# Kernel tuning notes

Hardware: AMD Instinct MI355X
Metric: run time of the kernel (lower is better)

Reference implementation:

```python
import jax, jax.numpy as jnp
import numpy as np

N = 50000      # nodes
E = 800000     # edges
D_IN = 128     # in_channels == hidden_channels
D_H = 128
R = 4          # num_relations
L = 3          # n_layers
D_MID = D_H // 4
D_OUT = 40
BN_EPS = 1e-5


def setup_inputs() -> dict:
    key = jax.random.key(0)
    ks = jax.random.split(key, 12)
    return {
        "x": jax.random.normal(ks[0], (N, D_IN), dtype=jnp.float32),
        "edge_index": jax.random.randint(ks[1], (2, E), 0, N, dtype=jnp.int64),
        "edge_type": jax.random.randint(ks[2], (E,), 0, R, dtype=jnp.int64),
        "W_skip": jax.random.normal(ks[3], (L, D_IN, D_H), dtype=jnp.float32) * 0.1,
        "W_film_skip": jax.random.normal(ks[4], (L, D_IN, 2 * D_H), dtype=jnp.float32) * 0.1,
        "W_rel": jax.random.normal(ks[5], (L, R, D_IN, D_H), dtype=jnp.float32) * 0.1,
        "W_film": jax.random.normal(ks[6], (L, R, D_IN, 2 * D_H), dtype=jnp.float32) * 0.1,
        "bn_w": jnp.ones((L, D_H), dtype=jnp.float32),
        "bn_b": jnp.zeros((L, D_H), dtype=jnp.float32),
        "lin1_w": jax.random.normal(ks[7], (D_H, D_MID), dtype=jnp.float32) * 0.1,
        "lin1_b": jnp.zeros((D_MID,), dtype=jnp.float32),
        "lin2_w": jax.random.normal(ks[8], (D_MID, D_OUT), dtype=jnp.float32) * 0.1,
        "lin2_b": jnp.zeros((D_OUT,), dtype=jnp.float32),
    }


def _film_conv(x, Wsk, Wfsk, Wr, Wf, src, dst, etype):
    # Self path: FiLM-modulated skip transform (PyG FiLMConv, act=ReLU).
    beta_s, gamma_s = jnp.split(x @ Wfsk, 2, axis=-1)  # split order: beta, gamma
    out = jax.nn.relu(gamma_s * (x @ Wsk) + beta_s)    # [N, D_H]
    # Per-relation node transforms (small GEMMs, avoids dynamic edge masking).
    xr = jnp.einsum('ni,rio->nro', x, Wr)              # [N, R, D_H]
    bg = jnp.einsum('ni,rio->nro', x, Wf)              # [N, R, 2*D_H]
    beta, gamma = jnp.split(bg, 2, axis=-1)            # each [N, R, D_H]
    # Messages: gamma_i * (W_r x_j) + beta_i, relation chosen per edge.
    msg = jax.nn.relu(gamma[dst, etype] * xr[src, etype] + beta[dst, etype])  # [E, D_H]
    # Mean aggregation per (target node, relation) subgraph, then sum relations.
    seg = dst * R + etype
    sums = jax.ops.segment_sum(msg, seg, num_segments=N * R)
    cnts = jax.ops.segment_sum(jnp.ones((msg.shape[0],), msg.dtype), seg, num_segments=N * R)
    mean = sums / jnp.maximum(cnts, 1.0)[:, None]      # [N*R, D_H]
    return out + mean.reshape(N, R, D_H).sum(axis=1)


def _batchnorm(h, w, b):
    mu = h.mean(axis=0)
    var = ((h - mu) ** 2).mean(axis=0)  # biased variance, as torch BN training
    return (h - mu) * jax.lax.rsqrt(var + BN_EPS) * w + b


def reference(x, edge_index, edge_type, W_skip, W_film_skip, W_rel, W_film,
              bn_w, bn_b, lin1_w, lin1_b, lin2_w, lin2_b):
    src, dst = edge_index[0], edge_index[1]
    h = x
    for l in range(L):
        h = _film_conv(h, W_skip[l], W_film_skip[l], W_rel[l], W_film[l], src, dst, edge_type)
        h = _batchnorm(h, bn_w[l], bn_b[l])
        # dropout treated as identity (deterministic reference)
    h = jax.nn.leaky_relu(h @ lin1_w + lin1_b, negative_slope=0.2)
    return h @ lin2_w + lin2_b
```

## Files before the change

### kernel.cpp

```cpp
#include <hip/hip_runtime.h>

#define N_NODES 50000
#define N_EDGES 800000
#define D 128
#define R_REL 4
#define L_LAYERS 3
#define M_SEG (N_NODES * R_REL)
#define NCOLS 384
#define BN_EPS 1e-5f

typedef unsigned short u16;
typedef __attribute__((ext_vector_type(8))) short short8v;
typedef __attribute__((ext_vector_type(4))) float f32x4;

static __device__ __forceinline__ u16 f2b(float f) {
    union { float f; unsigned int u; } a; a.f = f;
    unsigned int u = a.u;
    return (u16)((u + 0x7FFFu + ((u >> 16) & 1u)) >> 16);
}
static __device__ __forceinline__ float b2f(u16 b) {
    union { unsigned int u; float f; } a; a.u = ((unsigned int)b) << 16;
    return a.f;
}

__global__ void pack_w(const float* __restrict__ Wsk, const float* __restrict__ Wfsk,
                       const float* __restrict__ Wr, const float* __restrict__ Wf,
                       u16* __restrict__ Wpb) {
    int idx = blockIdx.x * 256 + threadIdx.x;
    if (idx >= L_LAYERS * 5 * NCOLS * D) return;
    int k = idx & 127;
    int rem = idx >> 7;
    int j = rem % NCOLS;
    int lp = rem / NCOLS;
    int l = lp / 5, p = lp % 5;
    float v;
    if (p == 0) {
        v = (j < D) ? Wsk[(l * D + k) * D + j] : Wfsk[(l * D + k) * 2 * D + (j - D)];
    } else {
        int r = p - 1;
        v = (j < D) ? Wr[((l * R_REL + r) * D + k) * D + j]
                    : Wf[((l * R_REL + r) * D + k) * 2 * D + (j - D)];
    }
    Wpb[idx] = f2b(v);
}

__global__ void cvt_bf16(const float* __restrict__ x, u16* __restrict__ xb) {
    int idx = blockIdx.x * 256 + threadIdx.x;
    if (idx >= N_NODES * D) return;
    xb[idx] = f2b(x[idx]);
}

__global__ void hist_k(const int* __restrict__ dst, const int* __restrict__ et, int* __restrict__ cnt) {
    int e = blockIdx.x * 256 + threadIdx.x;
    if (e >= N_EDGES) return;
    atomicAdd(&cnt[dst[e] * R_REL + et[e]], 1);
}

__global__ void scan_a(const int* __restrict__ cnt, int* __restrict__ bsum) {
    __shared__ int sm[256];
    int t = threadIdx.x;
    int idx = blockIdx.x * 256 + t;
    sm[t] = (idx < M_SEG) ? cnt[idx] : 0;
    __syncthreads();
    for (int s = 128; s > 0; s >>= 1) {
        if (t < s) sm[t] += sm[t + s];
        __syncthreads();
    }
    if (t == 0) bsum[blockIdx.x] = sm[0];
}

#define NB_SCAN 782
__global__ void scan_b(const int* __restrict__ bsum, int* __restrict__ bsumex, int* __restrict__ offs) {
    __shared__ int sm[1024];
    int t = threadIdx.x;
    int v = (t < NB_SCAN) ? bsum[t] : 0;
    sm[t] = v;
    __syncthreads();
    for (int d = 1; d < 1024; d <<= 1) {
        int add = (t >= d) ? sm[t - d] : 0;
        __syncthreads();
        sm[t] += add;
        __syncthreads();
    }
    if (t < NB_SCAN) bsumex[t] = sm[t] - v;
    if (t == NB_SCAN - 1) offs[M_SEG] = sm[t];
}

__global__ void scan_c(const int* __restrict__ cnt, const int* __restrict__ bsumex, int* __restrict__ offs) {
    __shared__ int sm[256];
    int t = threadIdx.x;
    int idx = blockIdx.x * 256 + t;
    int v = (idx < M_SEG) ? cnt[idx] : 0;
    sm[t] = v;
    __syncthreads();
    for (int d = 1; d < 256; d <<= 1) {
        int add = (t >= d) ? sm[t - d] : 0;
        __syncthreads();
        sm[t] += add;
        __syncthreads();
    }
    if (idx < M_SEG) offs[idx] = bsumex[blockIdx.x] + sm[t] - v;
}

__global__ void scatter_k(const int* __restrict__ src, const int* __restrict__ dst,
                          const int* __restrict__ et, const int* __restrict__ offs,
                          int* __restrict__ tmp, int* __restrict__ esrc) {
    int e = blockIdx.x * 256 + threadIdx.x;
    if (e >= N_EDGES) return;
    int seg = dst[e] * R_REL + et[e];
    int pos = offs[seg] + atomicAdd(&tmp[seg], 1);
    esrc[pos] = src[e];
}

__global__ __launch_bounds__(512) void gemm_mfma(const uint4* __restrict__ Aq,
                                                 const uint4* __restrict__ Bq,
                                                 u16* __restrict__ C) {
    __shared__ uint4 As[128 * 16];
    __shared__ uint4 Bs[128 * 16];
    int t = threadIdx.x;
    int m0 = blockIdx.x * 128;
    int n0 = blockIdx.y * 128;
#pragma unroll
    for (int i = 0; i < 4; ++i) {
        int idx = i * 512 + t;
        int row = idx >> 4, kk = idx & 15;
        int gr = m0 + row;
        if (gr >= N_NODES) gr = N_NODES - 1;
        As[(row << 4) + (kk ^ (row & 7))] = Aq[gr * 16 + kk];
        Bs[(row << 4) + (kk ^ (row & 7))] = Bq[(n0 + row) * 16 + kk];
    }
    __syncthreads();
    int lane = t & 63, w = t >> 6;
    int wr = w >> 2, wc = w & 3;
    int lr = lane & 15, lh = lane >> 4;
    f32x4 zero = {0.f, 0.f, 0.f, 0.f};
    f32x4 acc[4][2];
#pragma unroll
    for (int m = 0; m < 4; ++m)
#pragma unroll
        for (int n = 0; n < 2; ++n) acc[m][n] = zero;
#pragma unroll
    for (int ks = 0; ks < 4; ++ks) {
        short8v a[4], b[2];
#pragma unroll
        for (int m = 0; m < 4; ++m) {
            int row = wr * 64 + m * 16 + lr;
            a[m] = *reinterpret_cast<const short8v*>(&As[(row << 4) + ((ks * 4 + lh) ^ (row & 7))]);
        }
#pragma unroll
        for (int n = 0; n < 2; ++n) {
            int row = wc * 32 + n * 16 + lr;
            b[n] = *reinterpret_cast<const short8v*>(&Bs[(row << 4) + ((ks * 4 + lh) ^ (row & 7))]);
        }
#pragma unroll
        for (int m = 0; m < 4; ++m)
#pragma unroll
            for (int n = 0; n < 2; ++n)
                acc[m][n] = __builtin_amdgcn_mfma_f32_16x16x32_bf16(a[m], b[n], acc[m][n], 0, 0, 0);
    }
#pragma unroll
    for (int m = 0; m < 4; ++m) {
#pragma unroll
        for (int reg = 0; reg < 4; ++reg) {
            int gr = m0 + wr * 64 + m * 16 + lh * 4 + reg;
            if (gr < N_NODES) {
#pragma unroll
                for (int n = 0; n < 2; ++n) {
                    int col = n0 + wc * 32 + n * 16 + lr;
                    C[(size_t)gr * NCOLS + col] = f2b(acc[m][n][reg]);
                }
            }
        }
    }
}

__global__ __launch_bounds__(128) void film_agg(const u16* __restrict__ bufS,
                                                const u16* __restrict__ buf0, const u16* __restrict__ buf1,
                                                const u16* __restrict__ buf2, const u16* __restrict__ buf3,
                                                const int* __restrict__ offs, const int* __restrict__ esrc,
                                                float* __restrict__ acc) {
    int n = blockIdx.x, c = threadIdx.x;
    const u16* row = bufS + (size_t)n * NCOLS;
    float h = fmaxf(b2f(row[256 + c]) * b2f(row[c]) + b2f(row[128 + c]), 0.f);
    const u16* bufs[4] = {buf0, buf1, buf2, buf3};
#pragma unroll
    for (int r = 0; r < R_REL; ++r) {
        const u16* B = bufs[r];
        int seg = n * R_REL + r;
        int beg = offs[seg], end = offs[seg + 1];
        if (beg < end) {
            const u16* grow = B + (size_t)n * NCOLS;
            float g = b2f(grow[256 + c]), be = b2f(grow[128 + c]);
            float s = 0.f;
            for (int i = beg; i < end; ++i)
                s += fmaxf(g * b2f(B[(size_t)esrc[i] * NCOLS + c]) + be, 0.f);
            h += s / (float)(end - beg);
        }
    }
    acc[n * D + c] = h;
}

__global__ void film_self_b(const u16* __restrict__ buf, float* __restrict__ acc) {
    int idx = blockIdx.x * 256 + threadIdx.x;
    if (idx >= N_NODES * D) return;
    int n = idx >> 7, c = idx & 127;
    const u16* row = buf + (size_t)n * NCOLS;
    acc[idx] = fmaxf(b2f(row[256 + c]) * b2f(row[c]) + b2f(row[128 + c]), 0.f);
}

__global__ __launch_bounds__(128) void agg_rel_b(const u16* __restrict__ buf, const int* __restrict__ offs,
                                                 const int* __restrict__ esrc, float* __restrict__ acc, int r) {
    int n = blockIdx.x;
    int c = threadIdx.x;
    int seg = n * R_REL + r;
    int beg = offs[seg], end = offs[seg + 1];
    if (beg >= end) return;
    const u16* row = buf + (size_t)n * NCOLS;
    float g = b2f(row[256 + c]), be = b2f(row[128 + c]);
    float s = 0.f;
    for (int i = beg; i < end; ++i)
        s += fmaxf(g * b2f(buf[(size_t)esrc[i] * NCOLS + c]) + be, 0.f);
    acc[n * D + c] += s / (float)(end - beg);
}

__global__ __launch_bounds__(256) void bn_stats2(const float* __restrict__ acc, float* __restrict__ sums) {
    __shared__ float sm[256], sm2[256];
    int t = threadIdx.x;
    int c = t & 127, half = t >> 7;
    int rows = (N_NODES + gridDim.x - 1) / gridDim.x;
    int nb = blockIdx.x * rows;
    int n1 = min(nb + rows, N_NODES);
    float s = 0.f, s2 = 0.f;
    for (int n = nb + half; n < n1; n += 2) {
        float v = acc[n * D + c];
        s += v;
        s2 += v * v;
    }
    sm[t] = s; sm2[t] = s2;
    __syncthreads();
    if (t < 128) {
        atomicAdd(&sums[c], sm[t] + sm[t + 128]);
        atomicAdd(&sums[128 + c], sm2[t] + sm2[t + 128]);
    }
}

__global__ void bn_apply(const float* __restrict__ acc, const float* __restrict__ sums,
                         const float* __restrict__ w, const float* __restrict__ b,
                         u16* __restrict__ hb16) {
    int idx = blockIdx.x * 256 + threadIdx.x;
    if (idx >= N_NODES * D) return;
    int c = idx & 127;
    const float invn = 1.f / (float)N_NODES;
    float mu = sums[c] * invn;
    float var = sums[128 + c] * invn - mu * mu;
    float rs = rsqrtf(var + BN_EPS);
    hb16[idx] = f2b((acc[idx] - mu) * rs * w[c] + b[c]);
}

__global__ __launch_bounds__(128) void head_k(const u16* __restrict__ h, const float* __restrict__ w1,
                                              const float* __restrict__ b1, const float* __restrict__ w2,
                                              const float* __restrict__ b2, float* __restrict__ out) {
    __shared__ float hrow[128];
    __shared__ float part[128];
    __shared__ float mid[32];
    int n = blockIdx.x, t = threadIdx.x;
    hrow[t] = b2f(h[n * D + t]);
    __syncthreads();
    int m = t & 31, q = t >> 5;
    float p = 0.f;
#pragma unroll 8
    for (int k = q * 32; k < q * 32 + 32; ++k) p += hrow[k] * w1[k * 32 + m];
    part[t] = p;
    __syncthreads();
    if (t < 32) {
        float v = part[t] + part[t + 32] + part[t + 64] + part[t + 96] + b1[t];
        mid[t] = v > 0.f ? v : 0.2f * v;
    }
    __syncthreads();
    if (t < 40) {
        float o = b2[t];
#pragma unroll 8
        for (int mm = 0; mm < 32; ++mm) o += mid[mm] * w2[mm * 40 + t];
        out[n * 40 + t] = o;
    }
}

extern "C" void kernel_launch(void* const* d_in, const int* in_sizes, int n_in,
                              void* d_out, int out_size, void* d_ws, size_t ws_size,
                              hipStream_t stream) {
    const float* x    = (const float*)d_in[0];
    const int*   ei   = (const int*)d_in[1];
    const int*   et   = (const int*)d_in[2];
    const float* Wsk  = (const float*)d_in[3];
    const float* Wfsk = (const float*)d_in[4];
    const float* Wr   = (const float*)d_in[5];
    const float* Wf   = (const float*)d_in[6];
    const float* bnw  = (const float*)d_in[7];
    const float* bnb  = (const float*)d_in[8];
    const float* w1   = (const float*)d_in[9];
    const float* b1   = (const float*)d_in[10];
    const float* w2   = (const float*)d_in[11];
    const float* b2   = (const float*)d_in[12];
    const int* src = ei;
    const int* dst = ei + N_EDGES;

    char* ws = (char*)d_ws;
    size_t off = 0;
    auto alloc = [&](size_t bytes) -> void* {
        void* p = ws + off;
        off += (bytes + 255) & ~(size_t)255;
        return p;
    };
    const size_t BUF_B = (size_t)N_NODES * NCOLS * 2;
    u16*   Wpb  = (u16*)alloc((size_t)L_LAYERS * 5 * NCOLS * D * 2);
    u16*   inb  = (u16*)alloc((size_t)N_NODES * D * 2);
    float* acc  = (float*)alloc((size_t)N_NODES * D * 4);
    int*   cnt    = (int*)alloc((size_t)M_SEG * 4);
    int*   tmp    = (int*)alloc((size_t)M_SEG * 4);
    float* bns    = (float*)alloc((size_t)L_LAYERS * 256 * 4);
    int*   offs   = (int*)alloc((size_t)(M_SEG + 1) * 4);
    int*   esrc   = (int*)alloc((size_t)N_EDGES * 4);
    int*   bsum   = (int*)alloc(1024 * 4);
    int*   bsumex = (int*)alloc(1024 * 4);
    size_t base_off = off;
    bool big = (base_off + 5 * ((BUF_B + 255) & ~(size_t)255)) <= ws_size;
    u16* bufS = (u16*)alloc(BUF_B);
    u16* bufR[4];
    for (int r = 0; r < 4; ++r) bufR[r] = big ? (u16*)alloc(BUF_B) : bufS;

    hipMemsetAsync(cnt, 0, (size_t)M_SEG * 8 + (size_t)L_LAYERS * 1024, stream);

    pack_w<<<(L_LAYERS * 5 * NCOLS * D + 255) / 256, 256, 0, stream>>>(Wsk, Wfsk, Wr, Wf, Wpb);
    cvt_bf16<<<(N_NODES * D + 255) / 256, 256, 0, stream>>>(x, inb);
    hist_k<<<(N_EDGES + 255) / 256, 256, 0, stream>>>(dst, et, cnt);
    scan_a<<<NB_SCAN, 256, 0, stream>>>(cnt, bsum);
    scan_b<<<1, 1024, 0, stream>>>(bsum, bsumex, offs);
    scan_c<<<NB_SCAN, 256, 0, stream>>>(cnt, bsumex, offs);
    scatter_k<<<(N_EDGES + 255) / 256, 256, 0, stream>>>(src, dst, et, offs, tmp, esrc);

    const int nbm = (N_NODES + 127) / 128;
    for (int l = 0; l < L_LAYERS; ++l) {
        const uint4* Aq = (const uint4*)inb;
        const uint4* Wl = (const uint4*)(Wpb + (size_t)(l * 5) * NCOLS * D);
        if (big) {
            gemm_mfma<<<dim3(nbm, 3), 512, 0, stream>>>(Aq, Wl, bufS);
            for (int r = 0; r < R_REL; ++r)
                gemm_mfma<<<dim3(nbm, 3), 512, 0, stream>>>(
                    Aq, (const uint4*)(Wpb + (size_t)(l * 5 + 1 + r) * NCOLS * D), bufR[r]);
            film_agg<<<N_NODES, 128, 0, stream>>>(bufS, bufR[0], bufR[1], bufR[2], bufR[3], offs, esrc, acc);
        } else {
            gemm_mfma<<<dim3(nbm, 3), 512, 0, stream>>>(Aq, Wl, bufS);
            film_self_b<<<(N_NODES * D + 255) / 256, 256, 0, stream>>>(bufS, acc);
            for (int r = 0; r < R_REL; ++r) {
                gemm_mfma<<<dim3(nbm, 3), 512, 0, stream>>>(
                    Aq, (const uint4*)(Wpb + (size_t)(l * 5 + 1 + r) * NCOLS * D), bufS);
                agg_rel_b<<<N_NODES, 128, 0, stream>>>(bufS, offs, esrc, acc, r);
            }
        }
        bn_stats2<<<256, 256, 0, stream>>>(acc, bns + l * 256);
        bn_apply<<<(N_NODES * D + 255) / 256, 256, 0, stream>>>(acc, bns + l * 256, bnw + l * D, bnb + l * D, inb);
    }
    head_k<<<N_NODES, 128, 0, stream>>>(inb, w1, b1, w2, b2, (float*)d_out);
}
```

Measured before the change: 926.9 us.

## Merge five relation GEMMs into one launch and vectorize FiLM aggregation

New measurement: 836.1 us. 9.8% less time.

```diff
diff --git a/kernel.cpp b/kernel.cpp
--- a/kernel.cpp
+++ b/kernel.cpp
@@ -112,14 +112,13 @@
     esrc[pos] = src[e];
 }
 
-__global__ __launch_bounds__(512) void gemm_mfma(const uint4* __restrict__ Aq,
-                                                 const uint4* __restrict__ Bq,
-                                                 u16* __restrict__ C) {
+__global__ __launch_bounds__(512) void gemm5(const uint4* __restrict__ Aq,
+                                             const uint4* __restrict__ Bq,
+                                             u16* __restrict__ Call) {
     __shared__ uint4 As[128 * 16];
-    __shared__ uint4 Bs[128 * 16];
     int t = threadIdx.x;
     int m0 = blockIdx.x * 128;
-    int n0 = blockIdx.y * 128;
+    int p = blockIdx.y;
 #pragma unroll
     for (int i = 0; i < 4; ++i) {
         int idx = i * 512 + t;
@@ -127,100 +126,109 @@
         int gr = m0 + row;
         if (gr >= N_NODES) gr = N_NODES - 1;
         As[(row << 4) + (kk ^ (row & 7))] = Aq[gr * 16 + kk];
-        Bs[(row << 4) + (kk ^ (row & 7))] = Bq[(n0 + row) * 16 + kk];
     }
     __syncthreads();
     int lane = t & 63, w = t >> 6;
     int wr = w >> 2, wc = w & 3;
     int lr = lane & 15, lh = lane >> 4;
+    short8v a[4][4];
+#pragma unroll
+    for (int m = 0; m < 4; ++m) {
+        int row = wr * 64 + m * 16 + lr;
+#pragma unroll
+        for (int ks = 0; ks < 4; ++ks)
+            a[m][ks] = *reinterpret_cast<const short8v*>(&As[(row << 4) + ((ks * 4 + lh) ^ (row & 7))]);
+    }
+    const uint4* Bp = Bq + (size_t)p * NCOLS * 16;
+    u16* Cp = Call + (size_t)p * N_NODES * NCOLS;
     f32x4 zero = {0.f, 0.f, 0.f, 0.f};
-    f32x4 acc[4][2];
-#pragma unroll
-    for (int m = 0; m < 4; ++m)
-#pragma unroll
-        for (int n = 0; n < 2; ++n) acc[m][n] = zero;
-#pragma unroll
-    for (int ks = 0; ks < 4; ++ks) {
-        short8v a[4], b[2];
+#pragma unroll
+    for (int chunk = 0; chunk < 3; ++chunk) {
+        int n0 = chunk * 128;
+        f32x4 acc[4][2];
+#pragma unroll
+        for (int m = 0; m < 4; ++m)
+#pragma unroll
+            for (int n = 0; n < 2; ++n) acc[m][n] = zero;
+#pragma unroll
+        for (int ks = 0; ks < 4; ++ks) {
+            short8v b[2];
+#pragma unroll
+            for (int n = 0; n < 2; ++n) {
+                int row = n0 + wc * 32 + n * 16 + lr;
+                b[n] = *reinterpret_cast<const short8v*>(&Bp[row * 16 + ks * 4 + lh]);
+            }
+#pragma unroll
+            for (int m = 0; m < 4; ++m)
+#pragma unroll
+                for (int n = 0; n < 2; ++n)
+                    acc[m][n] = __builtin_amdgcn_mfma_f32_16x16x32_bf16(a[m][ks], b[n], acc[m][n], 0, 0, 0);
+        }
 #pragma unroll
         for (int m = 0; m < 4; ++m) {
-            int row = wr * 64 + m * 16 + lr;
-            a[m] = *reinterpret_cast<const short8v*>(&As[(row << 4) + ((ks * 4 + lh) ^ (row & 7))]);
-        }
-#pragma unroll
-        for (int n = 0; n < 2; ++n) {
-            int row = wc * 32 + n * 16 + lr;
-            b[n] = *reinterpret_cast<const short8v*>(&Bs[(row << 4) + ((ks * 4 + lh) ^ (row & 7))]);
-        }
-#pragma unroll
-        for (int m = 0; m < 4; ++m)
-#pragma unroll
-            for (int n = 0; n < 2; ++n)
-                acc[m][n] = __builtin_amdgcn_mfma_f32_16x16x32_bf16(a[m], b[n], acc[m][n], 0, 0, 0);
-    }
-#pragma unroll
-    for (int m = 0; m < 4; ++m) {
-#pragma unroll
-        for (int reg = 0; reg < 4; ++reg) {
-            int gr = m0 + wr * 64 + m * 16 + lh * 4 + reg;
-            if (gr < N_NODES) {
-#pragma unroll
-                for (int n = 0; n < 2; ++n) {
-                    int col = n0 + wc * 32 + n * 16 + lr;
-                    C[(size_t)gr * NCOLS + col] = f2b(acc[m][n][reg]);
+#pragma unroll
+            for (int reg = 0; reg < 4; ++reg) {
+                int gr = m0 + wr * 64 + m * 16 + lh * 4 + reg;
+                if (gr < N_NODES) {
+#pragma unroll
+                    for (int n = 0; n < 2; ++n) {
+                        int col = n0 + wc * 32 + n * 16 + lr;
+                        Cp[(size_t)gr * NCOLS + col] = f2b(acc[m][n][reg]);
+                    }
                 }
             }
         }
     }
 }
 
-__global__ __launch_bounds__(128) void film_agg(const u16* __restrict__ bufS,
-                                                const u16* __restrict__ buf0, const u16* __restrict__ buf1,
-                                                const u16* __restrict__ buf2, const u16* __restrict__ buf3,
-                                                const int* __restrict__ offs, const int* __restrict__ esrc,
-                                                float* __restrict__ acc) {
-    int n = blockIdx.x, c = threadIdx.x;
-    const u16* row = bufS + (size_t)n * NCOLS;
-    float h = fmaxf(b2f(row[256 + c]) * b2f(row[c]) + b2f(row[128 + c]), 0.f);
-    const u16* bufs[4] = {buf0, buf1, buf2, buf3};
+__global__ __launch_bounds__(256) void film_agg2(const u16* __restrict__ bufAll,
+                                                 const int* __restrict__ offs, const int* __restrict__ esrc,
+                                                 float* __restrict__ acc) {
+    int t = threadIdx.x;
+    int n = blockIdx.x * 4 + (t >> 6);
+    int lane = t & 63;
+    int cg = (lane & 31) * 4;
+    int half = lane >> 5;
+    const u16* rowS = bufAll + (size_t)n * NCOLS;
+    ushort4 xs = *reinterpret_cast<const ushort4*>(&rowS[cg]);
+    ushort4 bs = *reinterpret_cast<const ushort4*>(&rowS[128 + cg]);
+    ushort4 gs = *reinterpret_cast<const ushort4*>(&rowS[256 + cg]);
+    float h0 = fmaxf(b2f(gs.x) * b2f(xs.x) + b2f(bs.x), 0.f);
+    float h1 = fmaxf(b2f(gs.y) * b2f(xs.y) + b2f(bs.y), 0.f);
+    float h2 = fmaxf(b2f(gs.z) * b2f(xs.z) + b2f(bs.z), 0.f);
+    float h3 = fmaxf(b2f(gs.w) * b2f(xs.w) + b2f(bs.w), 0.f);
 #pragma unroll
     for (int r = 0; r < R_REL; ++r) {
-        const u16* B = bufs[r];
+        const u16* B = bufAll + (size_t)(1 + r) * N_NODES * NCOLS;
         int seg = n * R_REL + r;
         int beg = offs[seg], end = offs[seg + 1];
         if (beg < end) {
             const u16* grow = B + (size_t)n * NCOLS;
-            float g = b2f(grow[256 + c]), be = b2f(grow[128 + c]);
-            float s = 0.f;
-            for (int i = beg; i < end; ++i)
-                s += fmaxf(g * b2f(B[(size_t)esrc[i] * NCOLS + c]) + be, 0.f);
-            h += s / (float)(end - beg);
+            ushort4 b4 = *reinterpret_cast<const ushort4*>(&grow[128 + cg]);
+            ushort4 g4 = *reinterpret_cast<const ushort4*>(&grow[256 + cg]);
+            float g0 = b2f(g4.x), g1 = b2f(g4.y), g2 = b2f(g4.z), g3 = b2f(g4.w);
+            float be0 = b2f(b4.x), be1 = b2f(b4.y), be2 = b2f(b4.z), be3 = b2f(b4.w);
+            float s0 = 0.f, s1 = 0.f, s2 = 0.f, s3 = 0.f;
+            for (int i = beg + half; i < end; i += 2) {
+                int src = esrc[i];
+                ushort4 x4 = *reinterpret_cast<const ushort4*>(&B[(size_t)src * NCOLS + cg]);
+                s0 += fmaxf(g0 * b2f(x4.x) + be0, 0.f);
+                s1 += fmaxf(g1 * b2f(x4.y) + be1, 0.f);
+                s2 += fmaxf(g2 * b2f(x4.z) + be2, 0.f);
+                s3 += fmaxf(g3 * b2f(x4.w) + be3, 0.f);
+            }
+            s0 += __shfl_xor(s0, 32);
+            s1 += __shfl_xor(s1, 32);
+            s2 += __shfl_xor(s2, 32);
+            s3 += __shfl_xor(s3, 32);
+            float inv = 1.f / (float)(end - beg);
+            h0 += s0 * inv; h1 += s1 * inv; h2 += s2 * inv; h3 += s3 * inv;
         }
     }
-    acc[n * D + c] = h;
-}
-
-__global__ void film_self_b(const u16* __restrict__ buf, float* __restrict__ acc) {
-    int idx = blockIdx.x * 256 + threadIdx.x;
-    if (idx >= N_NODES * D) return;
-    int n = idx >> 7, c = idx & 127;
-    const u16* row = buf + (size_t)n * NCOLS;
-    acc[idx] = fmaxf(b2f(row[256 + c]) * b2f(row[c]) + b2f(row[128 + c]), 0.f);
-}
-
-__global__ __launch_bounds__(128) void agg_rel_b(const u16* __restrict__ buf, const int* __restrict__ offs,
-                                                 const int* __restrict__ esrc, float* __restrict__ acc, int r) {
-    int n = blockIdx.x;
-    int c = threadIdx.x;
-    int seg = n * R_REL + r;
-    int beg = offs[seg], end = offs[seg + 1];
-    if (beg >= end) return;
-    const u16* row = buf + (size_t)n * NCOLS;
-    float g = b2f(row[256 + c]), be = b2f(row[128 + c]);
-    float s = 0.f;
-    for (int i = beg; i < end; ++i)
-        s += fmaxf(g * b2f(buf[(size_t)esrc[i] * NCOLS + c]) + be, 0.f);
-    acc[n * D + c] += s / (float)(end - beg);
+    if (half == 0) {
+        float4 o = make_float4(h0, h1, h2, h3);
+        *reinterpret_cast<float4*>(&acc[(size_t)n * D + cg]) = o;
+    }
 }
 
 __global__ __launch_bounds__(256) void bn_stats2(const float* __restrict__ acc, float* __restrict__ sums) {
@@ -311,7 +319,6 @@
         off += (bytes + 255) & ~(size_t)255;
         return p;
     };
-    const size_t BUF_B = (size_t)N_NODES * NCOLS * 2;
     u16*   Wpb  = (u16*)alloc((size_t)L_LAYERS * 5 * NCOLS * D * 2);
     u16*   inb  = (u16*)alloc((size_t)N_NODES * D * 2);
     float* acc  = (float*)alloc((size_t)N_NODES * D * 4);
@@ -322,11 +329,7 @@
     int*   esrc   = (int*)alloc((size_t)N_EDGES * 4);
     int*   bsum   = (int*)alloc(1024 * 4);
     int*   bsumex = (int*)alloc(1024 * 4);
-    size_t base_off = off;
-    bool big = (base_off + 5 * ((BUF_B + 255) & ~(size_t)255)) <= ws_size;
-    u16* bufS = (u16*)alloc(BUF_B);
-    u16* bufR[4];
-    for (int r = 0; r < 4; ++r) bufR[r] = big ? (u16*)alloc(BUF_B) : bufS;
+    u16*   bufAll = (u16*)alloc((size_t)5 * N_NODES * NCOLS * 2);
 
     hipMemsetAsync(cnt, 0, (size_t)M_SEG * 8 + (size_t)L_LAYERS * 1024, stream);
 
@@ -340,23 +343,9 @@
 
     const int nbm = (N_NODES + 127) / 128;
     for (int l = 0; l < L_LAYERS; ++l) {
-        const uint4* Aq = (const uint4*)inb;
-        const uint4* Wl = (const uint4*)(Wpb + (size_t)(l * 5) * NCOLS * D);
-        if (big) {
-            gemm_mfma<<<dim3(nbm, 3), 512, 0, stream>>>(Aq, Wl, bufS);
-            for (int r = 0; r < R_REL; ++r)
-                gemm_mfma<<<dim3(nbm, 3), 512, 0, stream>>>(
-                    Aq, (const uint4*)(Wpb + (size_t)(l * 5 + 1 + r) * NCOLS * D), bufR[r]);
-            film_agg<<<N_NODES, 128, 0, stream>>>(bufS, bufR[0], bufR[1], bufR[2], bufR[3], offs, esrc, acc);
-        } else {
-            gemm_mfma<<<dim3(nbm, 3), 512, 0, stream>>>(Aq, Wl, bufS);
-            film_self_b<<<(N_NODES * D + 255) / 256, 256, 0, stream>>>(bufS, acc);
-            for (int r = 0; r < R_REL; ++r) {
-                gemm_mfma<<<dim3(nbm, 3), 512, 0, stream>>>(
-                    Aq, (const uint4*)(Wpb + (size_t)(l * 5 + 1 + r) * NCOLS * D), bufS);
-                agg_rel_b<<<N_NODES, 128, 0, stream>>>(bufS, offs, esrc, acc, r);
-            }
-        }
+        gemm5<<<dim3(nbm, 5), 512, 0, stream>>>((const uint4*)inb,
+                                                (const uint4*)(Wpb + (size_t)(l * 5) * NCOLS * D), bufAll);
+        film_agg2<<<N_NODES / 4, 256, 0, stream>>>(bufAll, offs, esrc, acc);
         bn_stats2<<<256, 256, 0, stream>>>(acc, bns + l * 256);
         bn_apply<<<(N_NODES * D + 255) / 256, 256, 0, stream>>>(acc, bns + l * 256, bnw + l * D, bnb + l * D, inb);
     }
```
